# Kernel tuning notes

Measured on AMD Instinct MI355X. Metric: run time of the kernel, lower is better.

The kernel has to match this reference:

```python
import jax, jax.numpy as jnp
import numpy as np

EMBED_DIM = 1024
NUM_HEADS = 8
PROJ_DIM = EMBED_DIM // NUM_HEADS  # 128
SIGMA = 1.0        # attn_param
DISP = 1           # attn_displacement
BATCH = 8
SEQ_LEN = 2048
# per-head hard-coded attention positions (length == num_heads)
POSITIONS = ['center', 'left', 'right', 'first', 'last', 'center', 'left', 'right']


def _head_centers(L):
    """Center of the analytic Gaussian per head and per query position. [H, L]"""
    i = jnp.arange(L, dtype=jnp.float32)
    centers = []
    for pos in POSITIONS:
        if pos == 'center':
            c = i
        elif pos == 'left':
            c = i - DISP
        elif pos == 'right':
            c = i + DISP
        elif pos == 'first':
            c = jnp.zeros_like(i)
        else:  # 'last' (no padding: last valid index is L-1)
            c = jnp.full_like(i, L - 1)
        centers.append(c)
    return jnp.stack(centers)  # [H, L]


def setup_inputs() -> dict:
    key = jax.random.key(0)
    k1, k2, k3 = jax.random.split(key, 3)
    x = jax.random.normal(k1, (BATCH, SEQ_LEN, EMBED_DIM), dtype=jnp.float32)
    # xavier-ish scale for square weights
    s = (6.0 / (EMBED_DIM + EMBED_DIM)) ** 0.5
    W_in = jax.random.uniform(k2, (EMBED_DIM, EMBED_DIM), dtype=jnp.float32, minval=-s, maxval=s)
    W_out = jax.random.uniform(k3, (EMBED_DIM, EMBED_DIM), dtype=jnp.float32, minval=-s, maxval=s)
    return {"x": x, "W_in": W_in, "W_out": W_out}


def reference(x, W_in, W_out):
    B, L, E = x.shape
    H, P = NUM_HEADS, PROJ_DIM
    # value projection (F.linear with input_weights), split into heads
    v = (x @ W_in.T).reshape(B, L, H, P).transpose(0, 2, 1, 3)  # [B, H, L, P]
    # analytic per-head attention weights: Gaussian in key-position around center
    j = jnp.arange(L, dtype=jnp.float32)
    c = _head_centers(L)                                         # [H, Lq]
    logits = -((j[None, None, :] - c[:, :, None]) ** 2) / (2.0 * SIGMA ** 2)  # [H, Lq, Lk]
    w = jax.nn.softmax(logits, axis=-1)                          # [H, Lq, Lk]
    # weighted value aggregation (torch.bmm(attn_weights, values) per head)
    attended = jnp.einsum('hqk,bhkp->bhqp', w, v)                # [B, H, L, P]
    attended = attended.transpose(0, 2, 1, 3).reshape(B, L, E)
    # bias-free output projection
    return attended @ W_out.T
```

## Files before the change

### kernel.cpp

```cpp
#include <hip/hip_runtime.h>
#include <stdint.h>

typedef unsigned short u16;
typedef unsigned int   u32;

typedef float  f32x4  __attribute__((ext_vector_type(4)));
typedef __bf16 bf16x8 __attribute__((ext_vector_type(8)));

__device__ __forceinline__ u16 f2bf(float f) {
  union { float f; u32 u; } c; c.f = f;
  u32 u = c.u + 0x7fffu + ((c.u >> 16) & 1u);
  return (u16)(u >> 16);
}
__device__ __forceinline__ float bf2f(u16 h) {
  union { u32 u; float f; } c; c.u = ((u32)h) << 16;
  return c.f;
}
__device__ __forceinline__ void gll16(const void* g, void* l) {
  __builtin_amdgcn_global_load_lds(
      (const __attribute__((address_space(1))) void*)g,
      (__attribute__((address_space(3))) void*)l, 16, 0, 0);
}

__global__ __launch_bounds__(256)
void cvt_all(const float4* __restrict__ x,  uint2* __restrict__ xb,  int n4x,
             const float4* __restrict__ wi, uint2* __restrict__ wib,
             const float4* __restrict__ wo, uint2* __restrict__ wob, int n4w) {
  int i = blockIdx.x * 256 + threadIdx.x;
  const float4* s; uint2* d; int j;
  if (i < n4x)            { s = x;  d = xb;  j = i; }
  else if (i < n4x + n4w) { s = wi; d = wib; j = i - n4x; }
  else                    { s = wo; d = wob; j = i - n4x - n4w; }
  float4 v = s[j];
  uint2 o;
  o.x = (u32)f2bf(v.x) | ((u32)f2bf(v.y) << 16);
  o.y = (u32)f2bf(v.z) | ((u32)f2bf(v.w) << 16);
  d[j] = o;
}

template <bool OUT_BF16>
__global__ __launch_bounds__(512, 2)
void gemm_nt_256(const u16* __restrict__ A, const u16* __restrict__ B,
                 void* __restrict__ Cout, int M, int N, int K) {
  __shared__ u16 Ls[65536];
  const int tid  = threadIdx.x;
  const int lane = tid & 63;
  const int wave = tid >> 6;
  const int wm   = wave >> 2;
  const int wn   = wave & 3;
  const int ml   = lane & 15;
  const int q    = lane >> 4;
  const int qx   = q ^ (ml & 3);
  const int hx   = (ml >> 2) & 1;

  const int flat = blockIdx.y * 4 + blockIdx.x;
  const int xcd  = flat & 7;
  const int slot = flat >> 3;
  const int mt   = xcd * (gridDim.y >> 3) + (slot >> 2);
  const int nt   = slot & 3;
  const int m0   = mt * 256;
  const int n0   = nt * 256;

  const int srr = tid >> 3;
  const int gc  = (tid & 7) ^ ((tid >> 3) & 7);
  const u16* Agb = A + (size_t)(m0 + srr) * K + gc * 8;
  const u16* Bgb = B + (size_t)(n0 + srr) * K + gc * 8;
  char* LsB = (char*)Ls;
  const int wlds = wave * 1024;

  auto stageAll = [&](int bufb, int k0) {
#pragma unroll
    for (int h = 0; h < 2; ++h) {
      char* d = LsB + bufb + h * 16384 + wlds;
      gll16(Agb + (size_t)(h * 128) * K + k0, d);
      gll16(Agb + (size_t)(h * 128 + 64) * K + k0, d + 8192);
    }
#pragma unroll
    for (int h = 0; h < 2; ++h) {
      char* d = LsB + bufb + 32768 + h * 16384 + wlds;
      gll16(Bgb + (size_t)(h * 128) * K + k0, d);
      gll16(Bgb + (size_t)(h * 128 + 64) * K + k0, d + 8192);
    }
  };

  const int aB_ = wm * 8192 + ml * 64 + qx * 8;
  const int bB_ = 16384 + (wn >> 1) * 8192 + ((wn & 1) * 64 + ml) * 64 + qx * 8;

  f32x4  acc[8][4] = {};
  bf16x8 af[4][2];
  bf16x8 bq[2][2][2];

  auto rdA = [&](int bw, int mh) {
#pragma unroll
    for (int i = 0; i < 4; ++i)
#pragma unroll
      for (int s = 0; s < 2; ++s)
        af[i][s] = *reinterpret_cast<const bf16x8*>(
            &Ls[bw + aB_ + mh * 4096 + i * 1024 + (s ^ hx) * 32]);
  };
  auto rdB = [&](int bw, int nh) {
#pragma unroll
    for (int j = 0; j < 2; ++j)
#pragma unroll
      for (int s = 0; s < 2; ++s)
        bq[nh][j][s] = *reinterpret_cast<const bf16x8*>(
            &Ls[bw + bB_ + nh * 2048 + j * 1024 + (s ^ hx) * 32]);
  };
  auto mfmaQ = [&](int mh, int nh) {
    __builtin_amdgcn_s_setprio(1);
#pragma unroll
    for (int s = 0; s < 2; ++s)
#pragma unroll
      for (int i = 0; i < 4; ++i)
#pragma unroll
        for (int j = 0; j < 2; ++j)
          acc[mh * 4 + i][nh * 2 + j] = __builtin_amdgcn_mfma_f32_16x16x32_bf16(
              af[i][s], bq[nh][j][s], acc[mh * 4 + i][nh * 2 + j], 0, 0, 0);
    __builtin_amdgcn_s_setprio(0);
  };

  stageAll(0, 0);
  asm volatile("s_waitcnt vmcnt(0)" ::: "memory");
  __builtin_amdgcn_s_barrier();

  const int NT = K >> 6;
  int bufb = 0;
  for (int t = 0; t < NT; ++t, bufb ^= 65536) {
    const int bw = bufb >> 1;
    rdA(bw, 0); rdB(bw, 0);
    if (t + 1 < NT) stageAll(bufb ^ 65536, (t + 1) << 6);
    __builtin_amdgcn_s_barrier();
    asm volatile("s_waitcnt lgkmcnt(0)" ::: "memory");
    mfmaQ(0, 0);
    __builtin_amdgcn_s_barrier();
    rdB(bw, 1);
    __builtin_amdgcn_s_barrier();
    asm volatile("s_waitcnt lgkmcnt(0)" ::: "memory");
    mfmaQ(0, 1);
    __builtin_amdgcn_s_barrier();
    rdA(bw, 1);
    __builtin_amdgcn_s_barrier();
    asm volatile("s_waitcnt lgkmcnt(0)" ::: "memory");
    mfmaQ(1, 1);
    __builtin_amdgcn_s_barrier();
    mfmaQ(1, 0);
    asm volatile("s_waitcnt vmcnt(0)" ::: "memory");
    __builtin_amdgcn_s_barrier();
  }

  const int rowb = m0 + wm * 128 + q * 4;
  const int colb = n0 + wn * 64 + ml;
#pragma unroll
  for (int mf = 0; mf < 8; ++mf)
#pragma unroll
    for (int nf = 0; nf < 4; ++nf)
#pragma unroll
      for (int r = 0; r < 4; ++r) {
        size_t idx = (size_t)(rowb + mf * 16 + r) * N + (colb + nf * 16);
        float val = acc[mf][nf][r];
        if (OUT_BF16) ((u16*)Cout)[idx] = f2bf(val);
        else          ((float*)Cout)[idx] = val;
      }
}

__global__ __launch_bounds__(256)
void gauss_conv(const u16* __restrict__ v, u16* __restrict__ att, int L) {
  constexpr float wt[13] = {
    1.5229979744712628e-08f, 3.7266531720786709e-06f, 3.3546262790251185e-04f,
    1.1108996538242306e-02f, 1.3533528323661270e-01f, 6.0653065971263342e-01f,
    1.0f,
    6.0653065971263342e-01f, 1.3533528323661270e-01f, 1.1108996538242306e-02f,
    3.3546262790251185e-04f, 3.7266531720786709e-06f, 1.5229979744712628e-08f
  };
  const int t  = threadIdx.x;
  const int fg = t & 15;
  const int li = t >> 4;
  const int l  = blockIdx.x * 16 + li;
  const int h  = blockIdx.y;
  const int b  = blockIdx.z;
  int c;
  switch (h) {
    case 0: case 5: c = l;     break;
    case 1: case 6: c = l - 1; break;
    case 2: case 7: c = l + 1; break;
    case 3:         c = 0;     break;
    default:        c = L - 1; break;
  }
  const int fbase = h * 128 + fg * 8;
  const u16* vb = v + (size_t)b * L * 1024 + fbase;

  float a[8] = {};
  float Z = 0.f;
#pragma unroll
  for (int d = -6; d <= 6; ++d) {
    int idx = c + d;
    bool ok = (idx >= 0) && (idx < L);
    int ic_ = idx < 0 ? 0 : (idx >= L ? L - 1 : idx);
    float w = ok ? wt[d + 6] : 0.f;
    Z += w;
    uint4 p = *reinterpret_cast<const uint4*>(vb + (size_t)ic_ * 1024);
    a[0] = fmaf(w, bf2f((u16)(p.x & 0xffffu)), a[0]);
    a[1] = fmaf(w, bf2f((u16)(p.x >> 16)),     a[1]);
    a[2] = fmaf(w, bf2f((u16)(p.y & 0xffffu)), a[2]);
    a[3] = fmaf(w, bf2f((u16)(p.y >> 16)),     a[3]);
    a[4] = fmaf(w, bf2f((u16)(p.z & 0xffffu)), a[4]);
    a[5] = fmaf(w, bf2f((u16)(p.z >> 16)),     a[5]);
    a[6] = fmaf(w, bf2f((u16)(p.w & 0xffffu)), a[6]);
    a[7] = fmaf(w, bf2f((u16)(p.w >> 16)),     a[7]);
  }
  float inv = 1.0f / Z;
  uint4 o;
  o.x = (u32)f2bf(a[0] * inv) | ((u32)f2bf(a[1] * inv) << 16);
  o.y = (u32)f2bf(a[2] * inv) | ((u32)f2bf(a[3] * inv) << 16);
  o.z = (u32)f2bf(a[4] * inv) | ((u32)f2bf(a[5] * inv) << 16);
  o.w = (u32)f2bf(a[6] * inv) | ((u32)f2bf(a[7] * inv) << 16);
  *reinterpret_cast<uint4*>(att + (size_t)(b * L + l) * 1024 + fbase) = o;
}

extern "C" void kernel_launch(void* const* d_in, const int* in_sizes, int n_in,
                              void* d_out, int out_size, void* d_ws, size_t ws_size,
                              hipStream_t stream) {
  const int Bb = 8, L = 2048, E = 1024;
  const int M = Bb * L, N = E, K = E;

  const float* x  = (const float*)d_in[0];
  const float* Wi = (const float*)d_in[1];
  const float* Wo = (const float*)d_in[2];
  float* out = (float*)d_out;

  size_t offV  = (size_t)M * E * 2;
  size_t offWi = offV + (size_t)M * E * 2;
  size_t offWo = offWi + (size_t)E * E * 2;
  size_t need  = offWo + (size_t)E * E * 2;
  if (ws_size < need) return;

  u16* xb  = (u16*)d_ws;
  u16* v   = (u16*)((char*)d_ws + offV);
  u16* wib = (u16*)((char*)d_ws + offWi);
  u16* wob = (u16*)((char*)d_ws + offWo);
  u16* att = xb;

  int n4x = M * E / 4, n4w = E * E / 4;
  int nblk = (n4x + 2 * n4w) / 256;
  cvt_all<<<nblk, 256, 0, stream>>>((const float4*)x, (uint2*)xb, n4x,
                                    (const float4*)Wi, (uint2*)wib,
                                    (const float4*)Wo, (uint2*)wob, n4w);

  dim3 gg(N / 256, M / 256);
  gemm_nt_256<true ><<<gg, 512, 0, stream>>>(xb,  wib, v,   M, N, K);
  gauss_conv<<<dim3(L / 16, 8, Bb), 256, 0, stream>>>(v, att, L);
  gemm_nt_256<false><<<gg, 512, 0, stream>>>(att, wob, out, M, N, K);
}
```

Measured before the change: 213.7 us.

## Replace double-buffered GEMM LDS with single buffer and per-quadrant refill

```diff
diff --git a/kernel.cpp b/kernel.cpp
--- a/kernel.cpp
+++ b/kernel.cpp
@@ -42,7 +42,7 @@
 __global__ __launch_bounds__(512, 2)
 void gemm_nt_256(const u16* __restrict__ A, const u16* __restrict__ B,
                  void* __restrict__ Cout, int M, int N, int K) {
-  __shared__ u16 Ls[65536];
+  __shared__ u16 Ls[32768];
   const int tid  = threadIdx.x;
   const int lane = tid & 63;
   const int wave = tid >> 6;
@@ -61,50 +61,47 @@
   const int m0   = mt * 256;
   const int n0   = nt * 256;
 
-  const int srr = tid >> 3;
-  const int gc  = (tid & 7) ^ ((tid >> 3) & 7);
-  const u16* Agb = A + (size_t)(m0 + srr) * K + gc * 8;
-  const u16* Bgb = B + (size_t)(n0 + srr) * K + gc * 8;
+  const int rl = tid >> 3;
+  const int gc = (tid & 7) ^ (rl & 7);
+  const u16* Abase = A + (size_t)m0 * K + gc * 8;
+  const u16* Bbase = B + (size_t)n0 * K + gc * 8;
   char* LsB = (char*)Ls;
   const int wlds = wave * 1024;
 
-  auto stageAll = [&](int bufb, int k0) {
-#pragma unroll
-    for (int h = 0; h < 2; ++h) {
-      char* d = LsB + bufb + h * 16384 + wlds;
-      gll16(Agb + (size_t)(h * 128) * K + k0, d);
-      gll16(Agb + (size_t)(h * 128 + 64) * K + k0, d + 8192);
-    }
-#pragma unroll
-    for (int h = 0; h < 2; ++h) {
-      char* d = LsB + bufb + 32768 + h * 16384 + wlds;
-      gll16(Bgb + (size_t)(h * 128) * K + k0, d);
-      gll16(Bgb + (size_t)(h * 128 + 64) * K + k0, d + 8192);
-    }
-  };
-
-  const int aB_ = wm * 8192 + ml * 64 + qx * 8;
-  const int bB_ = 16384 + (wn >> 1) * 8192 + ((wn & 1) * 64 + ml) * 64 + qx * 8;
+  auto stageA = [&](int u, int k0) {
+    char* d = LsB + u * 16384 + wlds;
+    gll16(Abase + (size_t)(u * 64 + rl) * K + k0, d);
+    gll16(Abase + (size_t)(u * 64 + rl + 128) * K + k0, d + 8192);
+  };
+  auto stageB = [&](int v, int k0) {
+    char* d = LsB + 32768 + v * 16384 + wlds;
+    const int g1 = (rl >> 5) * 64 + v * 32 + (rl & 31);
+    gll16(Bbase + (size_t)g1 * K + k0, d);
+    gll16(Bbase + (size_t)(g1 + 128) * K + k0, d + 8192);
+  };
+
+  const int aB_ = wm * 4096 + ml * 64 + qx * 8;
+  const int bB_ = 16384 + wn * 2048 + ml * 64 + qx * 8;
 
   f32x4  acc[8][4] = {};
   bf16x8 af[4][2];
   bf16x8 bq[2][2][2];
 
-  auto rdA = [&](int bw, int mh) {
+  auto rdA = [&](int mh) {
 #pragma unroll
     for (int i = 0; i < 4; ++i)
 #pragma unroll
       for (int s = 0; s < 2; ++s)
         af[i][s] = *reinterpret_cast<const bf16x8*>(
-            &Ls[bw + aB_ + mh * 4096 + i * 1024 + (s ^ hx) * 32]);
-  };
-  auto rdB = [&](int bw, int nh) {
+            &Ls[mh * 8192 + aB_ + i * 1024 + (s ^ hx) * 32]);
+  };
+  auto rdB = [&](int nh) {
 #pragma unroll
     for (int j = 0; j < 2; ++j)
 #pragma unroll
       for (int s = 0; s < 2; ++s)
         bq[nh][j][s] = *reinterpret_cast<const bf16x8*>(
-            &Ls[bw + bB_ + nh * 2048 + j * 1024 + (s ^ hx) * 32]);
+            &Ls[bB_ + nh * 8192 + j * 1024 + (s ^ hx) * 32]);
   };
   auto mfmaQ = [&](int mh, int nh) {
     __builtin_amdgcn_s_setprio(1);
@@ -119,32 +116,37 @@
     __builtin_amdgcn_s_setprio(0);
   };
 
-  stageAll(0, 0);
+  stageA(0, 0); stageB(0, 0); stageB(1, 0); stageA(1, 0);
   asm volatile("s_waitcnt vmcnt(0)" ::: "memory");
   __builtin_amdgcn_s_barrier();
 
   const int NT = K >> 6;
-  int bufb = 0;
-  for (int t = 0; t < NT; ++t, bufb ^= 65536) {
-    const int bw = bufb >> 1;
-    rdA(bw, 0); rdB(bw, 0);
-    if (t + 1 < NT) stageAll(bufb ^ 65536, (t + 1) << 6);
+  for (int t = 0; t < NT; ++t) {
+    const int  kn  = (t + 1) << 6;
+    const bool stg = (t + 1 < NT);
+    rdA(0); rdB(0);
     __builtin_amdgcn_s_barrier();
     asm volatile("s_waitcnt lgkmcnt(0)" ::: "memory");
     mfmaQ(0, 0);
-    __builtin_amdgcn_s_barrier();
-    rdB(bw, 1);
+    asm volatile("s_waitcnt vmcnt(2)" ::: "memory");
+    __builtin_amdgcn_s_barrier();
+    rdB(1);
+    if (stg) { stageA(0, kn); stageB(0, kn); }
     __builtin_amdgcn_s_barrier();
     asm volatile("s_waitcnt lgkmcnt(0)" ::: "memory");
     mfmaQ(0, 1);
-    __builtin_amdgcn_s_barrier();
-    rdA(bw, 1);
+    if (stg) { asm volatile("s_waitcnt vmcnt(4)" ::: "memory"); }
+    else     { asm volatile("s_waitcnt vmcnt(0)" ::: "memory"); }
+    __builtin_amdgcn_s_barrier();
+    rdA(1);
+    if (stg) stageB(1, kn);
     __builtin_amdgcn_s_barrier();
     asm volatile("s_waitcnt lgkmcnt(0)" ::: "memory");
     mfmaQ(1, 1);
     __builtin_amdgcn_s_barrier();
+    if (stg) stageA(1, kn);
     mfmaQ(1, 0);
-    asm volatile("s_waitcnt vmcnt(0)" ::: "memory");
+    asm volatile("s_waitcnt vmcnt(4)" ::: "memory");
     __builtin_amdgcn_s_barrier();
   }
 
```

After: 208.2 us. 1.03x faster.
